# Kernel optimization log

Hardware: AMD Instinct MI355X
Metric: run time of the kernel (lower is better)

The kernel has to match this reference:

```python
import jax, jax.numpy as jnp
import numpy as np

N, D, K = 65536, 256, 4096
EPS = 1e-5
DECAY = 0.99
BN_MOMENTUM = 0.1


def setup_inputs() -> dict:
    key = jax.random.key(0)
    k1, k2, k3, k4, k5, k6 = jax.random.split(key, 6)
    return {
        "x": jax.random.normal(k1, (N, D), dtype=jnp.float32),
        "embedding": jax.random.normal(k2, (K, D), dtype=jnp.float32),
        "ema_cluster_size": jnp.zeros((K,), dtype=jnp.float32),
        "ema_w": jax.random.normal(k3, (K, D), dtype=jnp.float32),
        "running_mean": jax.random.normal(k4, (D,), dtype=jnp.float32) * 0.1,
        "running_var": jax.random.uniform(k5, (D,), dtype=jnp.float32, minval=0.5, maxval=1.5),
    }


def reference(x, embedding, ema_cluster_size, ema_w, running_mean, running_var):
    n_batch = x.shape[0]
    num_embeddings = embedding.shape[0]

    # BatchNorm1d (training mode, affine=False): normalize with batch stats
    mean = jnp.mean(x, axis=0)                       # [D]
    var = jnp.mean((x - mean) ** 2, axis=0)          # biased var, [D]
    xn = (x - mean) / jnp.sqrt(var + EPS)            # [N, D]
    # running stat updates (torch uses unbiased var for running_var)
    new_running_mean = (1.0 - BN_MOMENTUM) * running_mean + BN_MOMENTUM * mean
    var_unbiased = var * (n_batch / (n_batch - 1.0))
    new_running_var = (1.0 - BN_MOMENTUM) * running_var + BN_MOMENTUM * var_unbiased

    # squared euclidean distances [N, K]
    distances = (jnp.sum(xn ** 2, axis=1, keepdims=True)
                 + jnp.sum(embedding ** 2, axis=1)
                 - 2.0 * xn @ embedding.T)
    idx = jnp.argmin(distances, axis=1)              # [N]

    # one-hot scatter stats via segment_sum (== encodings.T contractions)
    counts = jax.ops.segment_sum(jnp.ones((n_batch,), dtype=x.dtype), idx,
                                 num_segments=num_embeddings)   # [K]
    dw = jax.ops.segment_sum(xn, idx, num_segments=num_embeddings)  # [K, D]

    # EMA updates
    new_cs = ema_cluster_size * DECAY + (1.0 - DECAY) * counts
    n_total = jnp.sum(new_cs)
    new_cs = (new_cs + 1e-5) / (n_total + num_embeddings * 1e-5) * n_total
    new_ema_w = ema_w * DECAY + (1.0 - DECAY) * dw
    new_embedding = new_ema_w / new_cs[:, None]

    running_std = jnp.sqrt(new_running_var + EPS)
    embedding_output = new_embedding * running_std[None, :] + new_running_mean[None, :]

    return (idx[:, None], new_embedding, embedding_output, new_cs, new_ema_w,
            new_running_mean, new_running_var)
```

## Files before the change

kernel.cpp:

```cpp
#include <hip/hip_runtime.h>
#include <cfloat>
#include <cmath>

#define NROWS 65536
#define DDIM 256
#define KDIM 4096

typedef short bf16x8 __attribute__((ext_vector_type(8)));
typedef float f32x4 __attribute__((ext_vector_type(4)));

constexpr float EPSV = 1e-5f;
constexpr float DECAYV = 0.99f;
constexpr float MOMV = 0.1f;
constexpr float DELTA = 0.4f;
constexpr int CAP = 16;
constexpr int SEG = 128;

constexpr size_t WS_CNT     = 0;
constexpr size_t WS_NFLAG   = WS_CNT + NROWS;
constexpr size_t WS_HIST    = WS_NFLAG + 64;
constexpr size_t WS_ZEND    = WS_HIST + KDIM;
constexpr size_t WS_START   = WS_ZEND;
constexpr size_t WS_FILLPOS = WS_START + KDIM;
constexpr size_t WS_SEGSTART= WS_FILLPOS + KDIM;
constexpr size_t WS_NSEG    = WS_SEGSTART + KDIM + 64;
constexpr size_t WS_SEGLIST = WS_NSEG + 64;
constexpr size_t WS_PARTSUM = WS_SEGLIST + 4672;
constexpr size_t WS_PARTSQ  = WS_PARTSUM + 2048 * DDIM;
constexpr size_t WS_MIDSUM  = WS_PARTSQ + 2048 * DDIM;
constexpr size_t WS_MIDSQ   = WS_MIDSUM + 256 * DDIM;
constexpr size_t WS_MEAN    = WS_MIDSQ + 256 * DDIM;
constexpr size_t WS_RSTD    = WS_MEAN + DDIM;
constexpr size_t WS_NRMEAN  = WS_RSTD + DDIM;
constexpr size_t WS_NRVAR   = WS_NRMEAN + DDIM;
constexpr size_t WS_BVEC    = WS_NRVAR + DDIM;
constexpr size_t WS_NCSRAW  = WS_BVEC + KDIM;
constexpr size_t WS_NTOT    = WS_NCSRAW + KDIM;
constexpr size_t WS_ROWINFO = WS_NTOT + 64;
constexpr size_t WS_IDX     = WS_ROWINFO + 16 * (size_t)NROWS;
constexpr size_t WS_ROWTHR  = WS_IDX + NROWS;
constexpr size_t WS_FLAG    = WS_ROWTHR + NROWS;
constexpr size_t WS_ROWLIST = WS_FLAG + NROWS;
constexpr size_t WS_CAND    = WS_ROWLIST + NROWS;
constexpr size_t WS_DWPART  = WS_CAND;
constexpr size_t WS_EPROW   = WS_CAND + (size_t)NROWS * CAP;
constexpr size_t WS_EIMG    = WS_EPROW + (size_t)KDIM * DDIM;
constexpr size_t WS_XIMG    = WS_EIMG + 524288;

constexpr size_t O_IDX   = 0;
constexpr size_t O_EMB   = NROWS;
constexpr size_t O_EOUT  = O_EMB + (size_t)KDIM * DDIM;
constexpr size_t O_CS    = O_EOUT + (size_t)KDIM * DDIM;
constexpr size_t O_EMAW  = O_CS + KDIM;
constexpr size_t O_RMEAN = O_EMAW + (size_t)KDIM * DDIM;
constexpr size_t O_RVAR  = O_RMEAN + DDIM;

__device__ inline unsigned bfpack(float a, float b) {
    unsigned ua = __float_as_uint(a), ub = __float_as_uint(b);
    ua = (ua + 0x7FFFu + ((ua >> 16) & 1u)) >> 16;
    ub = (ub + 0x7FFFu + ((ub >> 16) & 1u)) & 0xFFFF0000u;
    return (ua & 0xFFFFu) | ub;
}

#define GLOAD_LDS16(g, l) __builtin_amdgcn_global_load_lds(                       \
        (const __attribute__((address_space(1))) void*)(g),                        \
        (__attribute__((address_space(3))) void*)(l), 16, 0, 0)

__global__ __launch_bounds__(128) void k_bnpack(const float* __restrict__ x,
                                                float* __restrict__ ws) {
    const int t = threadIdx.x;
    const int b = blockIdx.x;
    char* ximg = (char*)(ws + WS_XIMG);
    float s0 = 0.f, s1 = 0.f, q0 = 0.f, q1 = 0.f;
    const int r0 = b * 32;
#pragma unroll 4
    for (int i = 0; i < 32; ++i) {
        const int r = r0 + i;
        const float2 v = *(const float2*)(x + (size_t)r * DDIM + 2 * t);
        s0 += v.x; s1 += v.y; q0 += v.x * v.x; q1 += v.y * v.y;
        const int db = (4 * t + ((r & 15) << 5)) & 511;
        *(unsigned*)(ximg + (size_t)r * 512 + db) = bfpack(v.x, v.y);
    }
    *(float2*)(ws + WS_PARTSUM + (size_t)b * DDIM + 2 * t) = make_float2(s0, s1);
    *(float2*)(ws + WS_PARTSQ  + (size_t)b * DDIM + 2 * t) = make_float2(q0, q1);
}

__global__ __launch_bounds__(256) void k_bn_mid(float* __restrict__ ws) {
    const int d = threadIdx.x, j = blockIdx.x;
    float s = 0.f, q = 0.f;
#pragma unroll
    for (int i = 0; i < 8; ++i) {
        s += ws[WS_PARTSUM + (size_t)(j * 8 + i) * DDIM + d];
        q += ws[WS_PARTSQ  + (size_t)(j * 8 + i) * DDIM + d];
    }
    ws[WS_MIDSUM + (size_t)j * DDIM + d] = s;
    ws[WS_MIDSQ  + (size_t)j * DDIM + d] = q;
}

__global__ __launch_bounds__(256) void k_bn_final(const float* __restrict__ rmean_in,
                                                  const float* __restrict__ rvar_in,
                                                  float* __restrict__ ws,
                                                  float* __restrict__ out) {
    const int d = threadIdx.x;
    float s = 0.f, sq = 0.f;
    for (int b = 0; b < 256; ++b) {
        s  += ws[WS_MIDSUM + (size_t)b * DDIM + d];
        sq += ws[WS_MIDSQ  + (size_t)b * DDIM + d];
    }
    const float mean = s / (float)NROWS;
    float var = sq / (float)NROWS - mean * mean;
    var = fmaxf(var, 0.f);
    const float rstd = 1.0f / sqrtf(var + EPSV);
    const float nrm  = (1.0f - MOMV) * rmean_in[d] + MOMV * mean;
    const float varu = var * ((float)NROWS / (float)(NROWS - 1));
    const float nrv  = (1.0f - MOMV) * rvar_in[d] + MOMV * varu;
    ws[WS_MEAN + d] = mean;
    ws[WS_RSTD + d] = rstd;
    ws[WS_NRMEAN + d] = nrm;
    ws[WS_NRVAR + d] = nrv;
    out[O_RMEAN + d] = nrm;
    out[O_RVAR + d] = nrv;
}

__global__ __launch_bounds__(128) void k_eprime(const float* __restrict__ emb,
                                                float* __restrict__ ws) {
    __shared__ float red[128];
    const int k = blockIdx.x, t = threadIdx.x;
    const int d0 = 2 * t, d1 = 2 * t + 1;
    const float em0 = emb[(size_t)k * DDIM + d0], em1 = emb[(size_t)k * DDIM + d1];
    const float rs0 = ws[WS_RSTD + d0], rs1 = ws[WS_RSTD + d1];
    const float mn0 = ws[WS_MEAN + d0], mn1 = ws[WS_MEAN + d1];
    const float e0 = em0 * rs0, e1 = em1 * rs1;
    ws[WS_EPROW + (size_t)k * DDIM + d0] = e0;
    ws[WS_EPROW + (size_t)k * DDIM + d1] = e1;
    char* img = (char*)(ws + WS_EIMG);
    const int db = (4 * t + ((k & 15) << 5)) & 511;
    *(unsigned*)(img + (size_t)k * 512 + db) = bfpack(e0, e1);
    red[t] = em0 * em0 + 2.f * mn0 * e0 + em1 * em1 + 2.f * mn1 * e1;
    __syncthreads();
    for (int s = 64; s > 0; s >>= 1) { if (t < s) red[t] += red[t + s]; __syncthreads(); }
    if (t == 0) ws[WS_BVEC + k] = red[0];
}

__global__ __launch_bounds__(256, 3) void k_gemm_min(float* __restrict__ ws) {
    extern __shared__ char smem[];
    const int t = threadIdx.x, lane = t & 63, w = t >> 6;
    const int l4 = lane & 15, kg = lane >> 4;
    const int tile = blockIdx.x >> 2;
    const int cq   = blockIdx.x & 3;
    const int rowbase = tile * 128 + w * 32;
    const char* ximg = (const char*)(ws + WS_XIMG);
    const char* eimg = (const char*)(ws + WS_EIMG) + (size_t)cq * 524288;
    const float* bvec = ws + WS_BVEC;

    bf16x8 a[2][8];
#pragma unroll
    for (int m = 0; m < 2; ++m) {
        const char* rp = ximg + (size_t)(rowbase + m * 16 + l4) * 512;
#pragma unroll
        for (int ts = 0; ts < 8; ++ts) {
            const int byte = ((kg * 16 + ts * 64) + (l4 << 5)) & 511;
            a[m][ts] = *(const bf16x8*)(rp + byte);
        }
    }

    float b1v[2][4], b2v[2][4];
    int b1i[2][4];
#pragma unroll
    for (int m = 0; m < 2; ++m)
#pragma unroll
        for (int r = 0; r < 4; ++r) { b1v[m][r] = FLT_MAX; b2v[m][r] = FLT_MAX; b1i[m][r] = 0; }

#pragma unroll
    for (int rr = 0; rr < 4; ++rr) {
        const int off = rr * 4096 + w * 1024;
        GLOAD_LDS16(eimg + off + lane * 16, smem + off);
    }
    __syncthreads();

    for (int ch = 0; ch < 32; ++ch) {
        const char* cur = smem + (ch & 1) * 16384;
        if (ch + 1 < 32) {
            const char* src = eimg + (size_t)(ch + 1) * 16384;
            char* nb = smem + ((ch + 1) & 1) * 16384;
#pragma unroll
            for (int rr = 0; rr < 4; ++rr) {
                const int off = rr * 4096 + w * 1024;
                GLOAD_LDS16(src + off + lane * 16, nb + off);
            }
        }

        f32x4 acc[2][2];
#pragma unroll
        for (int m = 0; m < 2; ++m)
#pragma unroll
            for (int n = 0; n < 2; ++n) acc[m][n] = 0.f;

#pragma unroll
        for (int ts = 0; ts < 8; ++ts) {
            const int rot = ((kg * 16 + ts * 64) + (l4 << 5)) & 511;
            bf16x8 bfr[2];
#pragma unroll
            for (int n = 0; n < 2; ++n)
                bfr[n] = *(const bf16x8*)(cur + (n * 16 + l4) * 512 + rot);
#pragma unroll
            for (int m = 0; m < 2; ++m)
#pragma unroll
                for (int n = 0; n < 2; ++n)
                    acc[m][n] = __builtin_amdgcn_mfma_f32_16x16x32_bf16(a[m][ts], bfr[n], acc[m][n], 0, 0, 0);
        }

#pragma unroll
        for (int n = 0; n < 2; ++n) {
            const int col = cq * 1024 + ch * 32 + n * 16 + l4;
            const float bc = bvec[col];
#pragma unroll
            for (int m = 0; m < 2; ++m)
#pragma unroll
                for (int r = 0; r < 4; ++r) {
                    const float s = fmaf(-2.f, acc[m][n][r], bc);
                    const bool lt = s < b1v[m][r];
                    b2v[m][r] = lt ? b1v[m][r] : fminf(b2v[m][r], s);
                    b1i[m][r] = lt ? col : b1i[m][r];
                    b1v[m][r] = lt ? s : b1v[m][r];
                }
        }
        __syncthreads();
    }

    float4* rowinfo = (float4*)(ws + WS_ROWINFO);
#pragma unroll
    for (int m = 0; m < 2; ++m)
#pragma unroll
        for (int r = 0; r < 4; ++r) {
            float v1 = b1v[m][r], v2 = b2v[m][r];
            int i1 = b1i[m][r];
#pragma unroll
            for (int st = 1; st < 16; st <<= 1) {
                const float o1 = __shfl_xor(v1, st);
                const int   oi = __shfl_xor(i1, st);
                const float o2 = __shfl_xor(v2, st);
                const bool lt = o1 < v1;
                v2 = lt ? fminf(v1, o2) : fminf(v2, o1);
                i1 = lt ? oi : i1;
                v1 = fminf(v1, o1);
            }
            if (l4 == 0) {
                const int row = rowbase + m * 16 + kg * 4 + r;
                rowinfo[(size_t)row * 4 + cq] =
                    make_float4(v1, __int_as_float(i1), v2, 0.f);
            }
        }
}

__global__ __launch_bounds__(256) void k_flag(float* __restrict__ ws,
                                              float* __restrict__ out) {
    const int r = blockIdx.x * 256 + threadIdx.x;
    const float4* rowinfo = (const float4*)(ws + WS_ROWINFO);
    float v1 = FLT_MAX, v2 = FLT_MAX;
    int i1 = 0;
#pragma unroll
    for (int c = 0; c < 4; ++c) {
        const float4 p = rowinfo[(size_t)r * 4 + c];
        const float a = p.x, b = p.z;
        if (a < v1) { v2 = fminf(fminf(v1, b), v2); v1 = a; i1 = __float_as_int(p.y); }
        else        { v2 = fminf(v2, a); }
    }
    ws[WS_ROWTHR + r] = v1 + DELTA;
    if (v2 - v1 <= DELTA) {
        const int pos = atomicAdd((int*)(ws + WS_NFLAG), 1);
        ((int*)(ws + WS_FLAG))[pos] = r;
    } else {
        out[O_IDX + r] = (float)i1;
        ((int*)(ws + WS_IDX))[r] = i1;
    }
}

__global__ __launch_bounds__(256) void k_cand(float* __restrict__ ws) {
    extern __shared__ char smem[];
    const int t = threadIdx.x, lane = t & 63, w = t >> 6;
    const int l4 = lane & 15, kg = lane >> 4;
    const char* ximg = (const char*)(ws + WS_XIMG);
    const char* eimg0 = (const char*)(ws + WS_EIMG);
    const float* bvec = ws + WS_BVEC;
    const int* flag = (const int*)(ws + WS_FLAG);
    int* cnt = (int*)(ws + WS_CNT);
    int* cand = (int*)(ws + WS_CAND);
    const int nflag = *(const int*)(ws + WS_NFLAG);
    if (nflag == 0) return;
    const int ntiles = (nflag + 127) >> 7;
    const int nitems = ntiles * 8;

    for (int item = blockIdx.x; item < nitems; item += gridDim.x) {
        const int tile = item >> 3, slice = item & 7;
        const int base = tile * 128 + w * 32;
        const char* eimg = eimg0 + (size_t)slice * 262144;
        bf16x8 a[2][8];
        int frow[2][4];
        float thr[2][4];
#pragma unroll
        for (int m = 0; m < 2; ++m) {
            const int ia = base + m * 16 + l4;
            const int rowa = flag[ia < nflag ? ia : (nflag - 1)];
            const char* rp = ximg + (size_t)rowa * 512;
#pragma unroll
            for (int ts = 0; ts < 8; ++ts) {
                const int byte = ((kg * 16 + ts * 64) + ((rowa & 15) << 5)) & 511;
                a[m][ts] = *(const bf16x8*)(rp + byte);
            }
#pragma unroll
            for (int r = 0; r < 4; ++r) {
                const int ie = base + m * 16 + kg * 4 + r;
                const bool val = ie < nflag;
                const int rowe = flag[val ? ie : (nflag - 1)];
                frow[m][r] = rowe;
                thr[m][r] = val ? ws[WS_ROWTHR + rowe] : -FLT_MAX;
            }
        }
#pragma unroll
        for (int rr = 0; rr < 4; ++rr) {
            const int off = rr * 4096 + w * 1024;
            GLOAD_LDS16(eimg + off + lane * 16, smem + off);
        }
        __syncthreads();

        for (int ch = 0; ch < 16; ++ch) {
            const char* cur = smem + (ch & 1) * 16384;
            if (ch + 1 < 16) {
                const char* src = eimg + (size_t)(ch + 1) * 16384;
                char* nb = smem + ((ch + 1) & 1) * 16384;
#pragma unroll
                for (int rr = 0; rr < 4; ++rr) {
                    const int off = rr * 4096 + w * 1024;
                    GLOAD_LDS16(src + off + lane * 16, nb + off);
                }
            }
            f32x4 acc[2][2];
#pragma unroll
            for (int m = 0; m < 2; ++m)
#pragma unroll
                for (int n = 0; n < 2; ++n) acc[m][n] = 0.f;
#pragma unroll
            for (int ts = 0; ts < 8; ++ts) {
                const int rot = ((kg * 16 + ts * 64) + (l4 << 5)) & 511;
                bf16x8 bfr[2];
#pragma unroll
                for (int n = 0; n < 2; ++n)
                    bfr[n] = *(const bf16x8*)(cur + (n * 16 + l4) * 512 + rot);
#pragma unroll
                for (int m = 0; m < 2; ++m)
#pragma unroll
                    for (int n = 0; n < 2; ++n)
                        acc[m][n] = __builtin_amdgcn_mfma_f32_16x16x32_bf16(a[m][ts], bfr[n], acc[m][n], 0, 0, 0);
            }
#pragma unroll
            for (int n = 0; n < 2; ++n) {
                const int col = slice * 512 + ch * 32 + n * 16 + l4;
                const float bc = bvec[col];
#pragma unroll
                for (int m = 0; m < 2; ++m)
#pragma unroll
                    for (int r = 0; r < 4; ++r) {
                        const float s = fmaf(-2.f, acc[m][n][r], bc);
                        if (s <= thr[m][r]) {
                            const int rr2 = frow[m][r];
                            const int pos = atomicAdd(&cnt[rr2], 1);
                            if (pos < CAP) cand[(size_t)rr2 * CAP + pos] = col;
                        }
                    }
            }
            __syncthreads();
        }
    }
}

__global__ __launch_bounds__(256) void k_resolve_f(const float* __restrict__ x,
                                                   float* __restrict__ ws,
                                                   float* __restrict__ out) {
    const int t = threadIdx.x, lane = t & 63;
    const int gw = (blockIdx.x * 256 + t) >> 6;
    const int nflag = *(const int*)(ws + WS_NFLAG);
    const int* flag = (const int*)(ws + WS_FLAG);
    const int* cnt = (const int*)(ws + WS_CNT);
    const int* cand = (const int*)(ws + WS_CAND);
    const float* eprow = ws + WS_EPROW;
    const float* bvec = ws + WS_BVEC;
    int* idx_int = (int*)(ws + WS_IDX);
    for (int i = gw; i < nflag; i += 1024) {
        const int row = flag[i];
        const float4 xr = ((const float4*)(x + (size_t)row * DDIM))[lane];
        const int n = cnt[row];
        float bestv = FLT_MAX;
        int bestk = KDIM;
        if (n >= 1 && n <= CAP) {
            for (int c = 0; c < n; ++c) {
                const int k = cand[(size_t)row * CAP + c];
                const float4 er = ((const float4*)(eprow + (size_t)k * DDIM))[lane];
                float p = xr.x * er.x + xr.y * er.y + xr.z * er.z + xr.w * er.w;
                p += __shfl_xor(p, 32); p += __shfl_xor(p, 16); p += __shfl_xor(p, 8);
                p += __shfl_xor(p, 4);  p += __shfl_xor(p, 2);  p += __shfl_xor(p, 1);
                const float s = fmaf(-2.f, p, bvec[k]);
                if (s < bestv || (s == bestv && k < bestk)) { bestv = s; bestk = k; }
            }
        } else {
            for (int k = 0; k < KDIM; ++k) {
                const float4 er = ((const float4*)(eprow + (size_t)k * DDIM))[lane];
                float p = xr.x * er.x + xr.y * er.y + xr.z * er.z + xr.w * er.w;
                p += __shfl_xor(p, 32); p += __shfl_xor(p, 16); p += __shfl_xor(p, 8);
                p += __shfl_xor(p, 4);  p += __shfl_xor(p, 2);  p += __shfl_xor(p, 1);
                const float s = fmaf(-2.f, p, bvec[k]);
                if (s < bestv || (s == bestv && k < bestk)) { bestv = s; bestk = k; }
            }
        }
        if (lane == 0) { out[O_IDX + row] = (float)bestk; idx_int[row] = bestk; }
    }
}

__global__ __launch_bounds__(256) void k_hist(float* __restrict__ ws) {
    const int r = blockIdx.x * 256 + threadIdx.x;
    const int k = ((const int*)(ws + WS_IDX))[r];
    atomicAdd((int*)(ws + WS_HIST) + k, 1);
}

__global__ __launch_bounds__(256) void k_scan(float* __restrict__ ws) {
    __shared__ int lsum[256], lseg[256];
    const int t = threadIdx.x;
    const int* hist = (const int*)(ws + WS_HIST);
    int h[16];
    int s = 0, g = 0;
#pragma unroll
    for (int i = 0; i < 16; ++i) {
        h[i] = hist[t * 16 + i];
        s += h[i];
        g += (h[i] + SEG - 1) / SEG;
    }
    lsum[t] = s; lseg[t] = g;
    __syncthreads();
    int v = s, u = g;
    for (int off = 1; off < 256; off <<= 1) {
        const int av = (t >= off) ? lsum[t - off] : 0;
        const int au = (t >= off) ? lseg[t - off] : 0;
        __syncthreads();
        v += av; u += au;
        lsum[t] = v; lseg[t] = u;
        __syncthreads();
    }
    int runs = v - s, rung = u - g;
    int* start = (int*)(ws + WS_START);
    int* fillpos = (int*)(ws + WS_FILLPOS);
    int* segst = (int*)(ws + WS_SEGSTART);
#pragma unroll
    for (int i = 0; i < 16; ++i) {
        start[t * 16 + i] = runs;
        fillpos[t * 16 + i] = runs;
        segst[t * 16 + i] = rung;
        runs += h[i];
        rung += (h[i] + SEG - 1) / SEG;
    }
    if (t == 255) {
        segst[KDIM] = rung;
        *(int*)(ws + WS_NSEG) = rung;
    }
}

__global__ __launch_bounds__(256) void k_fill(float* __restrict__ ws) {
    const int r = blockIdx.x * 256 + threadIdx.x;
    const int k = ((const int*)(ws + WS_IDX))[r];
    const int pos = atomicAdd((int*)(ws + WS_FILLPOS) + k, 1);
    ((int*)(ws + WS_ROWLIST))[pos] = r;
}

__global__ __launch_bounds__(256) void k_segfill(float* __restrict__ ws) {
    const int k = blockIdx.x * 256 + threadIdx.x;
    const int* segst = (const int*)(ws + WS_SEGSTART);
    const int base = segst[k];
    const int ns = segst[k + 1] - base;
    int* seglist = (int*)(ws + WS_SEGLIST);
    for (int j = 0; j < ns; ++j) seglist[base + j] = (k << 10) | j;
}

__global__ __launch_bounds__(256) void k_gather_seg(const float* __restrict__ x,
                                                    float* __restrict__ ws) {
    const int b = blockIdx.x;
    if (b >= *(const int*)(ws + WS_NSEG)) return;
    const int e = ((const int*)(ws + WS_SEGLIST))[b];
    const int k = e >> 10, j = e & 1023;
    const int base = ((const int*)(ws + WS_START))[k];
    const int n = ((const int*)(ws + WS_HIST))[k];
    const int st = base + j * SEG;
    const int en = min(st + SEG, base + n);
    const int* rowlist = (const int*)(ws + WS_ROWLIST);
    const int d = threadIdx.x;
    float s0 = 0.f, s1 = 0.f, s2 = 0.f, s3 = 0.f;
    int i = st;
    for (; i + 3 < en; i += 4) {
        s0 += x[(size_t)rowlist[i]     * DDIM + d];
        s1 += x[(size_t)rowlist[i + 1] * DDIM + d];
        s2 += x[(size_t)rowlist[i + 2] * DDIM + d];
        s3 += x[(size_t)rowlist[i + 3] * DDIM + d];
    }
    for (; i < en; ++i) s0 += x[(size_t)rowlist[i] * DDIM + d];
    (ws + WS_DWPART)[(size_t)b * DDIM + d] = (s0 + s1) + (s2 + s3);
}

__global__ __launch_bounds__(256) void k_ema_cs(const float* __restrict__ cs_in,
                                                float* __restrict__ ws) {
    __shared__ float red[256];
    const int t = threadIdx.x;
    const int* hist = (const int*)(ws + WS_HIST);
    float part = 0.f;
    for (int k = t; k < KDIM; k += 256) {
        const float ncs = cs_in[k] * DECAYV + (1.0f - DECAYV) * (float)hist[k];
        ws[WS_NCSRAW + k] = ncs;
        part += ncs;
    }
    red[t] = part;
    __syncthreads();
    for (int s = 128; s > 0; s >>= 1) { if (t < s) red[t] += red[t + s]; __syncthreads(); }
    if (t == 0) ws[WS_NTOT] = red[0];
}

__global__ __launch_bounds__(256) void k_final(const float* __restrict__ ema_w,
                                               const float* __restrict__ ws,
                                               float* __restrict__ out) {
    const int k = blockIdx.x;
    const int d = threadIdx.x;
    const int* segst = (const int*)(ws + WS_SEGSTART);
    const int ss = segst[k];
    const int ns = segst[k + 1] - ss;
    const float* dwpart = ws + WS_DWPART;
    float a0 = 0.f, a1 = 0.f;
    int j = 0;
    for (; j + 1 < ns; j += 2) {
        a0 += dwpart[(size_t)(ss + j)     * DDIM + d];
        a1 += dwpart[(size_t)(ss + j + 1) * DDIM + d];
    }
    if (j < ns) a0 += dwpart[(size_t)(ss + j) * DDIM + d];
    const float dwsum = a0 + a1;
    const int n = ((const int*)(ws + WS_HIST))[k];
    const float ntot = ws[WS_NTOT];
    const float ncs  = (ws[WS_NCSRAW + k] + 1e-5f) / (ntot + (float)KDIM * 1e-5f) * ntot;
    const float mn   = ws[WS_MEAN + d];
    const float rs   = ws[WS_RSTD + d];
    const size_t e   = (size_t)k * DDIM + d;
    const float dw   = (dwsum - (float)n * mn) * rs;
    const float nw   = ema_w[e] * DECAYV + (1.0f - DECAYV) * dw;
    const float nemb = nw / ncs;
    const float eo   = nemb * sqrtf(ws[WS_NRVAR + d] + EPSV) + ws[WS_NRMEAN + d];
    out[O_EMB + e]  = nemb;
    out[O_EOUT + e] = eo;
    out[O_EMAW + e] = nw;
    if (d == 0) out[O_CS + k] = ncs;
}

extern "C" void kernel_launch(void* const* d_in, const int* in_sizes, int n_in,
                              void* d_out, int out_size, void* d_ws, size_t ws_size,
                              hipStream_t stream) {
    const float* x     = (const float*)d_in[0];
    const float* emb   = (const float*)d_in[1];
    const float* cs    = (const float*)d_in[2];
    const float* ema_w = (const float*)d_in[3];
    const float* rmean = (const float*)d_in[4];
    const float* rvar  = (const float*)d_in[5];
    float* out = (float*)d_out;
    float* ws  = (float*)d_ws;

    hipMemsetAsync(ws, 0, WS_ZEND * sizeof(float), stream);

    k_bnpack<<<2048, 128, 0, stream>>>(x, ws);
    k_bn_mid<<<256, 256, 0, stream>>>(ws);
    k_bn_final<<<1, 256, 0, stream>>>(rmean, rvar, ws, out);
    k_eprime<<<KDIM, 128, 0, stream>>>(emb, ws);

    constexpr int LDSB = 32768;
    k_gemm_min<<<2048, 256, LDSB, stream>>>(ws);
    k_flag<<<NROWS / 256, 256, 0, stream>>>(ws, out);
    k_cand<<<512, 256, LDSB, stream>>>(ws);
    k_resolve_f<<<256, 256, 0, stream>>>(x, ws, out);

    k_hist<<<NROWS / 256, 256, 0, stream>>>(ws);
    k_scan<<<1, 256, 0, stream>>>(ws);
    k_fill<<<NROWS / 256, 256, 0, stream>>>(ws);
    k_segfill<<<KDIM / 256, 256, 0, stream>>>(ws);
    k_gather_seg<<<4608, 256, 0, stream>>>(x, ws);
    k_ema_cs<<<1, 256, 0, stream>>>(cs, ws);
    k_final<<<KDIM, 256, 0, stream>>>(ema_w, ws, out);
}
```

Measured before the change: 321.1 us.

## Pack argmin index into float low bits and fuse histogram/scan/EMA kernels

The GEMM argmin epilogue now packs the column index into the low 12 mantissa bits of the distance and tracks best and second-best with fminf and fmed3, which drops the separate index registers and compare-selects. The per-row info shrinks from float4 to float2. Occupancy is raised to 4 blocks per SM. The histogram is folded into the flag and resolve kernels via atomics, and segment-list filling plus the EMA cluster-size reduction are merged into the scan kernel, removing three launches. Truncating the mantissa coarsens the distances, so DELTA is widened to 1.0, which sends more rows to the exact re-check path.

```diff
diff --git a/kernel.cpp b/kernel.cpp
--- a/kernel.cpp
+++ b/kernel.cpp
@@ -12,7 +12,7 @@
 constexpr float EPSV = 1e-5f;
 constexpr float DECAYV = 0.99f;
 constexpr float MOMV = 0.1f;
-constexpr float DELTA = 0.4f;
+constexpr float DELTA = 1.0f;
 constexpr int CAP = 16;
 constexpr int SEG = 128;
 
@@ -37,7 +37,7 @@
 constexpr size_t WS_NCSRAW  = WS_BVEC + KDIM;
 constexpr size_t WS_NTOT    = WS_NCSRAW + KDIM;
 constexpr size_t WS_ROWINFO = WS_NTOT + 64;
-constexpr size_t WS_IDX     = WS_ROWINFO + 16 * (size_t)NROWS;
+constexpr size_t WS_IDX     = WS_ROWINFO + 8 * (size_t)NROWS;
 constexpr size_t WS_ROWTHR  = WS_IDX + NROWS;
 constexpr size_t WS_FLAG    = WS_ROWTHR + NROWS;
 constexpr size_t WS_ROWLIST = WS_FLAG + NROWS;
@@ -60,6 +60,10 @@
     ua = (ua + 0x7FFFu + ((ua >> 16) & 1u)) >> 16;
     ub = (ub + 0x7FFFu + ((ub >> 16) & 1u)) & 0xFFFF0000u;
     return (ua & 0xFFFFu) | ub;
+}
+
+__device__ inline float unpackval(float p) {
+    return __uint_as_float(__float_as_uint(p) & 0xFFFFF000u);
 }
 
 #define GLOAD_LDS16(g, l) __builtin_amdgcn_global_load_lds(                       \
@@ -142,7 +146,7 @@
     if (t == 0) ws[WS_BVEC + k] = red[0];
 }
 
-__global__ __launch_bounds__(256, 3) void k_gemm_min(float* __restrict__ ws) {
+__global__ __launch_bounds__(256, 4) void k_gemm_min(float* __restrict__ ws) {
     extern __shared__ char smem[];
     const int t = threadIdx.x, lane = t & 63, w = t >> 6;
     const int l4 = lane & 15, kg = lane >> 4;
@@ -164,12 +168,11 @@
         }
     }
 
-    float b1v[2][4], b2v[2][4];
-    int b1i[2][4];
+    float b1f[2][4], b2f[2][4];
 #pragma unroll
     for (int m = 0; m < 2; ++m)
 #pragma unroll
-        for (int r = 0; r < 4; ++r) { b1v[m][r] = FLT_MAX; b2v[m][r] = FLT_MAX; b1i[m][r] = 0; }
+        for (int r = 0; r < 4; ++r) { b1f[m][r] = FLT_MAX; b2f[m][r] = FLT_MAX; }
 
 #pragma unroll
     for (int rr = 0; rr < 4; ++rr) {
@@ -212,43 +215,39 @@
 
 #pragma unroll
         for (int n = 0; n < 2; ++n) {
-            const int col = cq * 1024 + ch * 32 + n * 16 + l4;
+            const unsigned col = (unsigned)(cq * 1024 + ch * 32 + n * 16 + l4);
             const float bc = bvec[col];
 #pragma unroll
             for (int m = 0; m < 2; ++m)
 #pragma unroll
                 for (int r = 0; r < 4; ++r) {
                     const float s = fmaf(-2.f, acc[m][n][r], bc);
-                    const bool lt = s < b1v[m][r];
-                    b2v[m][r] = lt ? b1v[m][r] : fminf(b2v[m][r], s);
-                    b1i[m][r] = lt ? col : b1i[m][r];
-                    b1v[m][r] = lt ? s : b1v[m][r];
+                    const float p = __uint_as_float(
+                        (__float_as_uint(s) & 0xFFFFF000u) | col);
+                    b2f[m][r] = __builtin_amdgcn_fmed3f(p, b1f[m][r], b2f[m][r]);
+                    b1f[m][r] = fminf(p, b1f[m][r]);
                 }
         }
         __syncthreads();
     }
 
-    float4* rowinfo = (float4*)(ws + WS_ROWINFO);
+    float2* rowinfo = (float2*)(ws + WS_ROWINFO);
 #pragma unroll
     for (int m = 0; m < 2; ++m)
 #pragma unroll
         for (int r = 0; r < 4; ++r) {
-            float v1 = b1v[m][r], v2 = b2v[m][r];
-            int i1 = b1i[m][r];
+            float v1 = b1f[m][r], v2 = b2f[m][r];
 #pragma unroll
             for (int st = 1; st < 16; st <<= 1) {
                 const float o1 = __shfl_xor(v1, st);
-                const int   oi = __shfl_xor(i1, st);
                 const float o2 = __shfl_xor(v2, st);
-                const bool lt = o1 < v1;
-                v2 = lt ? fminf(v1, o2) : fminf(v2, o1);
-                i1 = lt ? oi : i1;
+                const float mm = fminf(v2, o2);
+                v2 = __builtin_amdgcn_fmed3f(v1, o1, mm);
                 v1 = fminf(v1, o1);
             }
             if (l4 == 0) {
                 const int row = rowbase + m * 16 + kg * 4 + r;
-                rowinfo[(size_t)row * 4 + cq] =
-                    make_float4(v1, __int_as_float(i1), v2, 0.f);
+                rowinfo[(size_t)row * 4 + cq] = make_float2(v1, v2);
             }
         }
 }
@@ -256,23 +255,26 @@
 __global__ __launch_bounds__(256) void k_flag(float* __restrict__ ws,
                                               float* __restrict__ out) {
     const int r = blockIdx.x * 256 + threadIdx.x;
-    const float4* rowinfo = (const float4*)(ws + WS_ROWINFO);
-    float v1 = FLT_MAX, v2 = FLT_MAX;
-    int i1 = 0;
-#pragma unroll
-    for (int c = 0; c < 4; ++c) {
-        const float4 p = rowinfo[(size_t)r * 4 + c];
-        const float a = p.x, b = p.z;
-        if (a < v1) { v2 = fminf(fminf(v1, b), v2); v1 = a; i1 = __float_as_int(p.y); }
-        else        { v2 = fminf(v2, a); }
-    }
-    ws[WS_ROWTHR + r] = v1 + DELTA;
-    if (v2 - v1 <= DELTA) {
+    const float2* rowinfo = (const float2*)(ws + WS_ROWINFO);
+    float2 q = rowinfo[(size_t)r * 4];
+    float v1 = q.x, v2 = q.y;
+#pragma unroll
+    for (int c = 1; c < 4; ++c) {
+        q = rowinfo[(size_t)r * 4 + c];
+        const float mm = fminf(v2, q.y);
+        v2 = __builtin_amdgcn_fmed3f(v1, q.x, mm);
+        v1 = fminf(v1, q.x);
+    }
+    const float v1v = unpackval(v1);
+    const int   i1  = (int)(__float_as_uint(v1) & 0xFFFu);
+    ws[WS_ROWTHR + r] = v1v + DELTA;
+    if (unpackval(v2) - v1v <= DELTA) {
         const int pos = atomicAdd((int*)(ws + WS_NFLAG), 1);
         ((int*)(ws + WS_FLAG))[pos] = r;
     } else {
         out[O_IDX + r] = (float)i1;
         ((int*)(ws + WS_IDX))[r] = i1;
+        atomicAdd((int*)(ws + WS_HIST) + i1, 1);
     }
 }
 
@@ -412,18 +414,18 @@
                 if (s < bestv || (s == bestv && k < bestk)) { bestv = s; bestk = k; }
             }
         }
-        if (lane == 0) { out[O_IDX + row] = (float)bestk; idx_int[row] = bestk; }
-    }
-}
-
-__global__ __launch_bounds__(256) void k_hist(float* __restrict__ ws) {
-    const int r = blockIdx.x * 256 + threadIdx.x;
-    const int k = ((const int*)(ws + WS_IDX))[r];
-    atomicAdd((int*)(ws + WS_HIST) + k, 1);
-}
-
-__global__ __launch_bounds__(256) void k_scan(float* __restrict__ ws) {
+        if (lane == 0) {
+            out[O_IDX + row] = (float)bestk;
+            idx_int[row] = bestk;
+            atomicAdd((int*)(ws + WS_HIST) + bestk, 1);
+        }
+    }
+}
+
+__global__ __launch_bounds__(256) void k_scan(const float* __restrict__ cs_in,
+                                              float* __restrict__ ws) {
     __shared__ int lsum[256], lseg[256];
+    __shared__ float redf[256];
     const int t = threadIdx.x;
     const int* hist = (const int*)(ws + WS_HIST);
     int h[16];
@@ -449,18 +451,30 @@
     int* start = (int*)(ws + WS_START);
     int* fillpos = (int*)(ws + WS_FILLPOS);
     int* segst = (int*)(ws + WS_SEGSTART);
+    int* seglist = (int*)(ws + WS_SEGLIST);
+    float emapart = 0.f;
 #pragma unroll
     for (int i = 0; i < 16; ++i) {
-        start[t * 16 + i] = runs;
-        fillpos[t * 16 + i] = runs;
-        segst[t * 16 + i] = rung;
+        const int k = t * 16 + i;
+        start[k] = runs;
+        fillpos[k] = runs;
+        segst[k] = rung;
+        const int ns = (h[i] + SEG - 1) / SEG;
+        for (int j = 0; j < ns; ++j) seglist[rung + j] = (k << 10) | j;
         runs += h[i];
-        rung += (h[i] + SEG - 1) / SEG;
+        rung += ns;
+        const float ncs = cs_in[k] * DECAYV + (1.0f - DECAYV) * (float)h[i];
+        ws[WS_NCSRAW + k] = ncs;
+        emapart += ncs;
     }
     if (t == 255) {
         segst[KDIM] = rung;
         *(int*)(ws + WS_NSEG) = rung;
     }
+    redf[t] = emapart;
+    __syncthreads();
+    for (int ss = 128; ss > 0; ss >>= 1) { if (t < ss) redf[t] += redf[t + ss]; __syncthreads(); }
+    if (t == 0) ws[WS_NTOT] = redf[0];
 }
 
 __global__ __launch_bounds__(256) void k_fill(float* __restrict__ ws) {
@@ -468,15 +482,6 @@
     const int k = ((const int*)(ws + WS_IDX))[r];
     const int pos = atomicAdd((int*)(ws + WS_FILLPOS) + k, 1);
     ((int*)(ws + WS_ROWLIST))[pos] = r;
-}
-
-__global__ __launch_bounds__(256) void k_segfill(float* __restrict__ ws) {
-    const int k = blockIdx.x * 256 + threadIdx.x;
-    const int* segst = (const int*)(ws + WS_SEGSTART);
-    const int base = segst[k];
-    const int ns = segst[k + 1] - base;
-    int* seglist = (int*)(ws + WS_SEGLIST);
-    for (int j = 0; j < ns; ++j) seglist[base + j] = (k << 10) | j;
 }
 
 __global__ __launch_bounds__(256) void k_gather_seg(const float* __restrict__ x,
@@ -503,23 +508,6 @@
     (ws + WS_DWPART)[(size_t)b * DDIM + d] = (s0 + s1) + (s2 + s3);
 }
 
-__global__ __launch_bounds__(256) void k_ema_cs(const float* __restrict__ cs_in,
-                                                float* __restrict__ ws) {
-    __shared__ float red[256];
-    const int t = threadIdx.x;
-    const int* hist = (const int*)(ws + WS_HIST);
-    float part = 0.f;
-    for (int k = t; k < KDIM; k += 256) {
-        const float ncs = cs_in[k] * DECAYV + (1.0f - DECAYV) * (float)hist[k];
-        ws[WS_NCSRAW + k] = ncs;
-        part += ncs;
-    }
-    red[t] = part;
-    __syncthreads();
-    for (int s = 128; s > 0; s >>= 1) { if (t < s) red[t] += red[t + s]; __syncthreads(); }
-    if (t == 0) ws[WS_NTOT] = red[0];
-}
-
 __global__ __launch_bounds__(256) void k_final(const float* __restrict__ ema_w,
                                                const float* __restrict__ ws,
                                                float* __restrict__ out) {
@@ -578,11 +566,8 @@
     k_cand<<<512, 256, LDSB, stream>>>(ws);
     k_resolve_f<<<256, 256, 0, stream>>>(x, ws, out);
 
-    k_hist<<<NROWS / 256, 256, 0, stream>>>(ws);
-    k_scan<<<1, 256, 0, stream>>>(ws);
+    k_scan<<<1, 256, 0, stream>>>(cs, ws);
     k_fill<<<NROWS / 256, 256, 0, stream>>>(ws);
-    k_segfill<<<KDIM / 256, 256, 0, stream>>>(ws);
     k_gather_seg<<<4608, 256, 0, stream>>>(x, ws);
-    k_ema_cs<<<1, 256, 0, stream>>>(cs, ws);
     k_final<<<KDIM, 256, 0, stream>>>(ema_w, ws, out);
 }
```

Result: no change. 325.4 us (+1.3%).
